# Optimization experiments

Measured on AMD Instinct MI355X. Metric: run time of the kernel, lower is better.

Reference implementation:

```python
import jax, jax.numpy as jnp
import numpy as np

B, SP, SH, H = 32, 256, 256, 512
D = 2 * H       # input feature dim (2*hidden_size)
E = H // 2      # per-liner output dim
FD = 4 * H      # fusion linear dim
EPS = 1e-13


def setup_inputs() -> dict:
    key = jax.random.key(0)
    ks = jax.random.split(key, 8)
    s = 0.02
    return dict(
        premise_batch=jax.random.normal(ks[0], (B, SP, D), jnp.float32),
        hypothesis_batch=jax.random.normal(ks[1], (B, SH, D), jnp.float32),
        premise_mask=jax.random.randint(ks[2], (B, SP), 0, 2).astype(jnp.int32),
        hypothesis_mask=jax.random.randint(ks[3], (B, SH), 0, 2).astype(jnp.int32),
        W8=jax.random.normal(ks[4], (8, D, E), jnp.float32) * s,   # liner1..8 weights (in,out)
        B8=jnp.zeros((8, E), jnp.float32),
        Wl=jax.random.normal(ks[5], (8 * E, FD), jnp.float32) * s,  # self.liner
        bl=jnp.zeros((FD,), jnp.float32),
        Wp=jax.random.normal(ks[6], (7 * D, H), jnp.float32) * s,   # self._projection
        bp=jnp.zeros((H,), jnp.float32),
    )


def masked_softmax(logits, mask):
    # ESIM-style: multiply logits by mask, softmax, re-mask, renormalize.
    m = mask[:, None, :]                        # (b,1,kv)
    r = jax.nn.softmax(logits * m, axis=-1) * m
    return r / (r.sum(axis=-1, keepdims=True) + EPS)


def fuse(x, imp_self, imp_inter, W8, B8, Wl, bl):
    # x: (b,s,D); imp_*: (b,s,1). Eight modulated views -> liner1..8 -> concat -> liner+ReLU.
    a1 = imp_self * imp_inter
    a2 = imp_self + imp_inter
    a3 = jnp.maximum(imp_self, imp_inter)
    x1 = x * imp_self
    x2 = x * imp_inter
    mx = jnp.maximum(x1, x2)
    feats = jnp.stack([x * a1, x * a2, x * a3, mx,
                       x * (a1 + 1.0), x * (a2 + 1.0), x * (a3 + 1.0), mx + x], 0)  # (8,b,s,D)
    h = jnp.einsum('kbsd,kde->kbse', feats, W8) + B8[:, None, None, :]              # (8,b,s,E)
    cat = jnp.moveaxis(h, 0, 2).reshape(x.shape[0], x.shape[1], 8 * E)              # concat order 1..8
    return jax.nn.relu(cat @ Wl + bl)           # dropout is identity in eval mode


def reference(premise_batch, hypothesis_batch, premise_mask, hypothesis_mask,
              W8, B8, Wl, bl, Wp, bp):
    pm = premise_mask.astype(jnp.float32)
    hm = hypothesis_mask.astype(jnp.float32)
    scale = 1.0 / jnp.sqrt(jnp.float32(premise_batch.shape[-1]))

    sim = jnp.einsum('bpd,bhd->bph', premise_batch, hypothesis_batch) * scale
    ph = masked_softmax(sim, hm)                               # (b,Sp,Sh)
    hp = masked_softmax(sim.transpose(0, 2, 1), pm)            # (b,Sh,Sp)
    att_p = jnp.einsum('bph,bhd->bpd', ph, hypothesis_batch) * pm[:, :, None]
    att_h = jnp.einsum('bhp,bpd->bhd', hp, premise_batch) * hm[:, :, None]

    sp_attn = jax.nn.softmax(jnp.einsum('bpd,bqd->bpq', premise_batch, premise_batch) * scale, axis=-1)
    sh_attn = jax.nn.softmax(jnp.einsum('bpd,bqd->bpq', hypothesis_batch, hypothesis_batch) * scale, axis=-1)
    self_p = sp_attn @ premise_batch
    self_h = sh_attn @ hypothesis_batch

    imp_p = sp_attn.sum(axis=-2)[..., None]        # (b,Sp,1)
    imp_h = sh_attn.sum(axis=-2)[..., None]        # (b,Sh,1)
    inter_imp_h = ph.sum(axis=-2)[..., None]       # (b,Sh,1)
    inter_imp_p = hp.sum(axis=-2)[..., None]       # (b,Sp,1)

    p_all = fuse(premise_batch, imp_p, inter_imp_p, W8, B8, Wl, bl)
    h_all = fuse(hypothesis_batch, imp_h, inter_imp_h, W8, B8, Wl, bl)

    enh_p = jnp.concatenate([premise_batch, att_p, self_p, p_all,
                             premise_batch * att_p, premise_batch - att_p], axis=-1)
    enh_h = jnp.concatenate([hypothesis_batch, att_h, self_h, h_all,
                             hypothesis_batch * att_h, hypothesis_batch - att_h], axis=-1)
    out_p = jax.nn.relu(enh_p @ Wp + bp)
    out_h = jax.nn.relu(enh_h @ Wp + bp)
    return out_p, out_h
```

## Files before the change

kernel.cpp:

```cpp
#include <hip/hip_runtime.h>
#include <hip/hip_bf16.h>
#include <cmath>

#define BB 32
#define SS 256
#define DD 1024
#define EE 256
#define FDIM 2048
#define HH 512
#define KOUT6 (6 * 1024)
#define NROW (BB * SS)
#define NROW2 (2 * NROW)

static constexpr float SCALE = 1.0f / 32.0f;
static constexpr float EPSF  = 1e-13f;

typedef __attribute__((ext_vector_type(8))) short bf16x8;
typedef __attribute__((ext_vector_type(4))) float f32x4;

__device__ inline float4 ld4(const float* p) { return *(const float4*)p; }
__device__ inline ushort f2b(float f) {
    uint x = __float_as_uint(f);
    x += 0x7fffu + ((x >> 16) & 1u);
    return (ushort)(x >> 16);
}
__device__ inline float b2f(ushort u) { return __uint_as_float(((uint)u) << 16); }
__device__ inline bf16x8 cvt8(const float* v) {
    bf16x8 r;
#pragma unroll
    for (int j = 0; j < 8; ++j) r[j] = (short)f2b(v[j]);
    return r;
}
__device__ inline void b2f8(bf16x8 v, float* o) {
#pragma unroll
    for (int j = 0; j < 8; ++j) o[j] = b2f((ushort)v[j]);
}
__device__ inline bf16x8 ldf8(const float* p) {
    const float4 u0 = ld4(p), u1 = ld4(p + 4);
    float v[8] = {u0.x, u0.y, u0.z, u0.w, u1.x, u1.y, u1.z, u1.w};
    return cvt8(v);
}

__device__ inline int swz_orig_2d() {
    const int n   = blockIdx.y * gridDim.x + blockIdx.x;
    const int tot = gridDim.x * gridDim.y;
    return (n & 7) * (tot >> 3) + (n >> 3);
}
__device__ inline int swz_orig_3d() {
    const int n   = (blockIdx.z * gridDim.y + blockIdx.y) * gridDim.x + blockIdx.x;
    const int tot = gridDim.x * gridDim.y * gridDim.z;
    return (n & 7) * (tot >> 3) + (n >> 3);
}

__global__ __launch_bounds__(256)
void tpose_cvt_k(const float* __restrict__ in, ushort* __restrict__ out,
                 int K, int N, size_t inStride, size_t outStride) {
    __shared__ float T[32][33];
    const float* ib = in  + (size_t)blockIdx.z * inStride;
    ushort*      ob = out + (size_t)blockIdx.z * outStride;
    const int k0 = blockIdx.x * 32, n0 = blockIdx.y * 32;
    const int tx = threadIdx.x & 31, ty = threadIdx.x >> 5;
#pragma unroll
    for (int i = 0; i < 4; ++i) T[ty + 8 * i][tx] = ib[(size_t)(k0 + ty + 8 * i) * N + n0 + tx];
    __syncthreads();
#pragma unroll
    for (int i = 0; i < 4; ++i)
        ob[(size_t)(n0 + ty + 8 * i) * K + k0 + tx] = f2b(T[tx][ty + 8 * i]);
}

__global__ __launch_bounds__(256)
void tpose_wp_k(const float* __restrict__ Wp, ushort* __restrict__ out) {
    __shared__ float T[32][33];
    const int k0 = blockIdx.x * 32, n0 = blockIdx.y * 32;
    const int tx = threadIdx.x & 31, ty = threadIdx.x >> 5;
#pragma unroll
    for (int i = 0; i < 4; ++i) {
        const int k = k0 + ty + 8 * i, n = n0 + tx;
        float v = Wp[(size_t)k * HH + n];
        if (k < DD)           v += Wp[(size_t)(k + 6 * DD) * HH + n];
        else if (k < 2 * DD)  v -= Wp[(size_t)(k + 5 * DD) * HH + n];
        T[ty + 8 * i][tx] = v;
    }
    __syncthreads();
#pragma unroll
    for (int i = 0; i < 4; ++i)
        out[(size_t)(n0 + ty + 8 * i) * KOUT6 + k0 + tx] = f2b(T[tx][ty + 8 * i]);
}

__global__ __launch_bounds__(256)
void prep_xprod_k(const float* __restrict__ P, const float* __restrict__ H,
                  const ushort* __restrict__ attAb,
                  ushort* __restrict__ Xb, ushort* __restrict__ prodb) {
    const int idx = blockIdx.x * 256 + threadIdx.x;
    const int row = idx >> 7, chunk = idx & 127;
    const size_t off = (size_t)row * DD + chunk * 8;
    const float* X = (row < NROW) ? (P + off) : (H + off - (size_t)NROW * DD);
    const float4 x0 = ld4(X), x1 = ld4(X + 4);
    float xv[8] = {x0.x, x0.y, x0.z, x0.w, x1.x, x1.y, x1.z, x1.w};
    float av[8];
    b2f8(*(const bf16x8*)&attAb[off], av);
    float pv[8];
#pragma unroll
    for (int j = 0; j < 8; ++j) pv[j] = xv[j] * av[j];
    *(bf16x8*)&Xb[off]    = cvt8(xv);
    *(bf16x8*)&prodb[off] = cvt8(pv);
}

__global__ __launch_bounds__(256)
void reduce_out_k(float* __restrict__ out, const float* __restrict__ p1,
                  const float* __restrict__ bp) {
    const int gid = blockIdx.x * 256 + threadIdx.x;
    const size_t o = (size_t)gid * 4;
    const float4 a = ld4(&out[o]);
    const float4 b = ld4(&p1[o]);
    const float4 bv = ld4(&bp[(int)(o & 511)]);
    *(float4*)&out[o] = make_float4(fmaxf(a.x + b.x + bv.x, 0.f),
                                    fmaxf(a.y + b.y + bv.y, 0.f),
                                    fmaxf(a.z + b.z + bv.z, 0.f),
                                    fmaxf(a.w + b.w + bv.w, 0.f));
}

__global__ __launch_bounds__(256)
void softmax4_k(float* __restrict__ simPH, float* __restrict__ simPHT,
                float* __restrict__ simPP, float* __restrict__ simHH,
                const int* __restrict__ pma, const int* __restrict__ hma) {
    const int job = blockIdx.y;
    float* buf = job == 0 ? simPH : job == 1 ? simPHT : job == 2 ? simPP : simHH;
    const int* mask = job == 0 ? hma : job == 1 ? pma : nullptr;
    __shared__ float  redm[4];
    __shared__ float2 reds[4];
    const int row = blockIdx.x;
    const int b   = row >> 8;
    const int j   = threadIdx.x;
    const float v = buf[(size_t)row * SS + j];
    float mj = 1.0f, z = v;
    if (mask) { mj = (float)mask[b * SS + j]; z = v * mj; }
    float M = z;
#pragma unroll
    for (int off = 1; off < 64; off <<= 1) M = fmaxf(M, __shfl_xor(M, off));
    const int wid = j >> 6;
    if ((j & 63) == 0) redm[wid] = M;
    __syncthreads();
    M = fmaxf(fmaxf(redm[0], redm[1]), fmaxf(redm[2], redm[3]));
    const float e = expf(z - M);
    const float r = e * mj;
    float sz = e, sr = r;
#pragma unroll
    for (int off = 1; off < 64; off <<= 1) {
        sz += __shfl_xor(sz, off);
        sr += __shfl_xor(sr, off);
    }
    if ((j & 63) == 0) reds[wid] = make_float2(sz, sr);
    __syncthreads();
    const float Z  = reds[0].x + reds[1].x + reds[2].x + reds[3].x;
    const float Sm = reds[0].y + reds[1].y + reds[2].y + reds[3].y;
    buf[(size_t)row * SS + j] = mask ? (r / (Sm + EPSF * Z)) : (e / Z);
}

__global__ __launch_bounds__(256)
void colsum4_k(const float* __restrict__ spA, const float* __restrict__ shA,
               const float* __restrict__ hp, const float* __restrict__ ph,
               float* __restrict__ impS, float* __restrict__ impI) {
    const int job = blockIdx.y, b = blockIdx.x, j = threadIdx.x;
    const float* src = job == 0 ? spA : job == 1 ? shA : job == 2 ? hp : ph;
    float* dst = job == 0 ? impS : job == 1 ? impS + NROW : job == 2 ? impI : impI + NROW;
    const float* Mb = src + (size_t)b * SS * SS;
    float s = 0.f;
    for (int i = 0; i < SS; ++i) s += Mb[i * SS + j];
    dst[b * SS + j] = s;
}

#define LSWZ(kg, r) ((r) ^ ((kg) << 1))

#define MFMA_CORE()                                                                  \
    {                                                                                \
        bf16x8 afr[4], bfr[4];                                                       \
        _Pragma("unroll") for (int m = 0; m < 4; ++m)                                \
            afr[m] = *(const bf16x8*)As[kq][LSWZ(kq, wr + m * 16 + fr)];             \
        _Pragma("unroll") for (int n = 0; n < 4; ++n)                                \
            bfr[n] = *(const bf16x8*)Bs[kq][LSWZ(kq, wc + n * 16 + fr)];             \
        _Pragma("unroll") for (int m = 0; m < 4; ++m)                                \
            _Pragma("unroll") for (int n = 0; n < 4; ++n)                            \
                acc[m][n] = __builtin_amdgcn_mfma_f32_16x16x32_bf16(                 \
                    afr[m], bfr[n], acc[m][n], 0, 0, 0);                             \
    }

#define MFMA_PREAMBLE()                                                              \
    const int tid = threadIdx.x;                                                     \
    const int lane = tid & 63;                                                       \
    const int w = tid >> 6;                                                          \
    const int wr = (w >> 1) * 64, wc = (w & 1) * 64;                                 \
    const int fr = lane & 15;                                                        \
    const int kq = lane >> 4;                                                        \
    const int rq = kq * 4;                                                           \
    f32x4 acc[4][4] = {};

__global__ __launch_bounds__(256)
void mfma_nt_k(const float* __restrict__ P, const float* __restrict__ H,
               float* __restrict__ simPH, float* __restrict__ simPHT,
               float* __restrict__ simPP, float* __restrict__ simHH) {
    __shared__ __align__(16) ushort As[4][128][8];
    __shared__ __align__(16) ushort Bs[4][128][8];
    int orig = swz_orig_3d();
    const int cb = orig & 1; orig >>= 1;
    const int rb = orig & 1; orig >>= 1;
    const int g = orig >> 5, b = orig & 31;
    const float* Au = ((g == 2) ? H : P) + (size_t)b * SS * DD;
    const float* Bu = ((g == 1) ? P : H) + (size_t)b * SS * DD;
    const int col0 = cb * 128, row0 = rb * 128;
    MFMA_PREAMBLE();
    for (int k0 = 0; k0 < DD; k0 += 32) {
        bf16x8 ar[2], br[2];
#pragma unroll
        for (int i = 0; i < 2; ++i) {
            const int cid = tid + i * 256, srow = cid >> 2, skc = (cid & 3) * 8;
            ar[i] = ldf8(&Au[(size_t)(row0 + srow) * DD + k0 + skc]);
            br[i] = ldf8(&Bu[(size_t)(col0 + srow) * DD + k0 + skc]);
        }
        __syncthreads();
#pragma unroll
        for (int i = 0; i < 2; ++i) {
            const int cid = tid + i * 256, kg = cid & 3, rr = LSWZ(kg, cid >> 2);
            *(bf16x8*)As[kg][rr] = ar[i];
            *(bf16x8*)Bs[kg][rr] = br[i];
        }
        __syncthreads();
        MFMA_CORE();
    }
    float* Cb = (g == 0 ? simPH : g == 1 ? simPP : simHH) + (size_t)b * SS * SS;
#pragma unroll
    for (int m = 0; m < 4; ++m)
#pragma unroll
        for (int n = 0; n < 4; ++n) {
            const int c = col0 + wc + n * 16 + fr;
            const int r0 = row0 + wr + m * 16 + rq;
#pragma unroll
            for (int r = 0; r < 4; ++r) Cb[(size_t)(r0 + r) * SS + c] = acc[m][n][r] * SCALE;
            if (g == 0) {
                float* Tb = simPHT + (size_t)b * SS * SS;
                *(float4*)&Tb[(size_t)c * SS + r0] =
                    make_float4(acc[m][n][0] * SCALE, acc[m][n][1] * SCALE,
                                acc[m][n][2] * SCALE, acc[m][n][3] * SCALE);
            }
        }
}

__global__ __launch_bounds__(256)
void mfma_att_k(const float* __restrict__ ph, const float* __restrict__ hp,
                const float* __restrict__ spA, const float* __restrict__ shA,
                const ushort* __restrict__ PbT, const ushort* __restrict__ HbT,
                const int* __restrict__ pma, const int* __restrict__ hma,
                ushort* __restrict__ attAb, ushort* __restrict__ selfAb) {
    __shared__ __align__(16) ushort As[4][128][8];
    __shared__ __align__(16) ushort Bs[4][128][8];
    int orig = swz_orig_3d();
    const int x = orig & 7; orig >>= 3;
    const int y = orig & 1; orig >>= 1;
    const int g = orig >> 5, b = orig & 31;
    const float*  W  = (g == 0 ? ph : g == 1 ? hp : g == 2 ? spA : shA) + (size_t)b * SS * SS;
    const ushort* BT = ((g == 0 || g == 3) ? HbT : PbT) + (size_t)b * DD * SS;
    const int* rmask = g == 0 ? pma + b * SS : g == 1 ? hma + b * SS : nullptr;
    const int side = (g == 1 || g == 3);
    ushort* Ob = (g < 2 ? attAb : selfAb) + ((size_t)side * NROW + (size_t)b * SS) * DD;
    const int col0 = x * 128, row0 = y * 128;
    MFMA_PREAMBLE();
    for (int k0 = 0; k0 < SS; k0 += 32) {
        bf16x8 ar[2], br[2];
#pragma unroll
        for (int i = 0; i < 2; ++i) {
            const int cid = tid + i * 256, srow = cid >> 2, skc = (cid & 3) * 8;
            ar[i] = ldf8(&W[(size_t)(row0 + srow) * SS + k0 + skc]);
            br[i] = *(const bf16x8*)&BT[(size_t)(col0 + srow) * SS + k0 + skc];
        }
        __syncthreads();
#pragma unroll
        for (int i = 0; i < 2; ++i) {
            const int cid = tid + i * 256, kg = cid & 3, rr = LSWZ(kg, cid >> 2);
            *(bf16x8*)As[kg][rr] = ar[i];
            *(bf16x8*)Bs[kg][rr] = br[i];
        }
        __syncthreads();
        MFMA_CORE();
    }
#pragma unroll
    for (int m = 0; m < 4; ++m)
#pragma unroll
        for (int n = 0; n < 4; ++n) {
            const int c = col0 + wc + n * 16 + fr;
#pragma unroll
            for (int r = 0; r < 4; ++r) {
                const int rr = row0 + wr + m * 16 + rq + r;
                const float mm = rmask ? (float)rmask[rr] : 1.0f;
                Ob[(size_t)rr * DD + c] = f2b(acc[m][n][r] * mm);
            }
        }
}

__global__ __launch_bounds__(256)
void mfma_fuse_k(const float* __restrict__ P, const float* __restrict__ H,
                 const float* __restrict__ impS, const float* __restrict__ impI,
                 const ushort* __restrict__ W8T, const float* __restrict__ B8v,
                 ushort* __restrict__ catb) {
    __shared__ __align__(16) ushort As[4][128][8];
    __shared__ __align__(16) ushort Bs[4][128][8];
    const int orig = swz_orig_2d();
    const int cb = orig & 15, rb = orig >> 4;
    const int kf = cb >> 1, e0 = (cb & 1) * 128, row0 = rb * 128;
    const float* X = (row0 < NROW) ? P : H;
    const int rbase = (row0 < NROW) ? row0 : row0 - NROW;
    MFMA_PREAMBLE();
    const ushort* Wk = W8T + (size_t)kf * EE * DD;

    int srow_[2]; float sA[2], iA[2], cf[2];
#pragma unroll
    for (int i = 0; i < 2; ++i) {
        const int cid = tid + i * 256;
        srow_[i] = cid >> 2;
        const float s_ = impS[row0 + srow_[i]], i_ = impI[row0 + srow_[i]];
        sA[i] = s_; iA[i] = i_;
        float c = 0.f;
        switch (kf) {
            case 0: c = s_ * i_;             break;
            case 1: c = s_ + i_;             break;
            case 2: c = fmaxf(s_, i_);       break;
            case 4: c = s_ * i_ + 1.f;       break;
            case 5: c = s_ + i_ + 1.f;       break;
            case 6: c = fmaxf(s_, i_) + 1.f; break;
            default: break;
        }
        cf[i] = c;
    }
    for (int k0 = 0; k0 < DD; k0 += 32) {
        bf16x8 ar[2], br[2];
#pragma unroll
        for (int i = 0; i < 2; ++i) {
            const int cid = tid + i * 256, skc = (cid & 3) * 8;
            const float* src = &X[(size_t)(rbase + srow_[i]) * DD + k0 + skc];
            const float4 u0 = ld4(src), u1 = ld4(src + 4);
            float v[8] = {u0.x, u0.y, u0.z, u0.w, u1.x, u1.y, u1.z, u1.w};
            if (kf == 3) {
#pragma unroll
                for (int j = 0; j < 8; ++j) v[j] = fmaxf(v[j] * sA[i], v[j] * iA[i]);
            } else if (kf == 7) {
#pragma unroll
                for (int j = 0; j < 8; ++j) v[j] = fmaxf(v[j] * sA[i], v[j] * iA[i]) + v[j];
            } else {
#pragma unroll
                for (int j = 0; j < 8; ++j) v[j] *= cf[i];
            }
            ar[i] = cvt8(v);
            br[i] = *(const bf16x8*)&Wk[(size_t)(e0 + srow_[i]) * DD + k0 + skc];
        }
        __syncthreads();
#pragma unroll
        for (int i = 0; i < 2; ++i) {
            const int cid = tid + i * 256, kg = cid & 3, rr = LSWZ(kg, cid >> 2);
            *(bf16x8*)As[kg][rr] = ar[i];
            *(bf16x8*)Bs[kg][rr] = br[i];
        }
        __syncthreads();
        MFMA_CORE();
    }
#pragma unroll
    for (int m = 0; m < 4; ++m)
#pragma unroll
        for (int n = 0; n < 4; ++n) {
            const int el = e0 + wc + n * 16 + fr;
            const float bv = B8v[kf * EE + el];
#pragma unroll
            for (int r = 0; r < 4; ++r) {
                const int rr = row0 + wr + m * 16 + rq + r;
                catb[(size_t)rr * FDIM + kf * EE + el] = f2b(acc[m][n][r] + bv);
            }
        }
}

__global__ __launch_bounds__(256)
void mfma_lin_k(const ushort* __restrict__ A, const ushort* __restrict__ BT,
                const float* __restrict__ bias, ushort* __restrict__ C) {
    __shared__ __align__(16) ushort As[4][128][8];
    __shared__ __align__(16) ushort Bs[4][128][8];
    const int orig = swz_orig_2d();
    const int col0 = (orig & 15) * 128, row0 = (orig >> 4) * 128;
    MFMA_PREAMBLE();
    for (int k0 = 0; k0 < FDIM; k0 += 32) {
        bf16x8 ar[2], br[2];
#pragma unroll
        for (int i = 0; i < 2; ++i) {
            const int cid = tid + i * 256, srow = cid >> 2, skc = (cid & 3) * 8;
            ar[i] = *(const bf16x8*)&A [(size_t)(row0 + srow) * FDIM + k0 + skc];
            br[i] = *(const bf16x8*)&BT[(size_t)(col0 + srow) * FDIM + k0 + skc];
        }
        __syncthreads();
#pragma unroll
        for (int i = 0; i < 2; ++i) {
            const int cid = tid + i * 256, kg = cid & 3, rr = LSWZ(kg, cid >> 2);
            *(bf16x8*)As[kg][rr] = ar[i];
            *(bf16x8*)Bs[kg][rr] = br[i];
        }
        __syncthreads();
        MFMA_CORE();
    }
#pragma unroll
    for (int m = 0; m < 4; ++m)
#pragma unroll
        for (int n = 0; n < 4; ++n) {
            const int c = col0 + wc + n * 16 + fr;
            const float bv = bias[c];
#pragma unroll
            for (int r = 0; r < 4; ++r) {
                const int rr = row0 + wr + m * 16 + rq + r;
                C[(size_t)rr * FDIM + c] = f2b(fmaxf(acc[m][n][r] + bv, 0.f));
            }
        }
}

__device__ inline void out_seg(int k0, const ushort* Xb, const ushort* attAb,
                               const ushort* selfAb, const ushort* pallb,
                               const ushort* prodb,
                               const ushort*& seg, int& pitch, int& kloc) {
    switch (k0 >> 10) {
        case 0:  seg = Xb;     pitch = DD;   kloc = k0;          break;
        case 1:  seg = attAb;  pitch = DD;   kloc = k0 - DD;     break;
        case 2:  seg = selfAb; pitch = DD;   kloc = k0 - 2 * DD; break;
        case 3:
        case 4:  seg = pallb;  pitch = FDIM; kloc = k0 - 3 * DD; break;
        default: seg = prodb;  pitch = DD;   kloc = k0 - 5 * DD; break;
    }
}

__global__ __launch_bounds__(256)
void mfma_out_k(const ushort* __restrict__ Xb, const ushort* __restrict__ attAb,
                const ushort* __restrict__ selfAb, const ushort* __restrict__ pallb,
                const ushort* __restrict__ prodb, const ushort* __restrict__ WpT,
                const float* __restrict__ bp, float* __restrict__ dst0,
                float* __restrict__ dst1, int kchunk, int finalize) {
    __shared__ __align__(16) ushort As[4][128][8];
    __shared__ __align__(16) ushort Bs[4][128][8];
    int orig = swz_orig_3d();
    const int x = orig & 3; orig >>= 2;
    const int y = orig & 127; orig >>= 7;
    const int z = orig;
    const int col0 = x * 128, row0 = y * 128;
    const int kbase = z * kchunk;
    float* dst = z == 0 ? dst0 : dst1;
    MFMA_PREAMBLE();
    for (int t = 0; t < kchunk / 32; ++t) {
        const int k0 = kbase + t * 32;
        const ushort* seg; int pitch, kloc;
        out_seg(k0, Xb, attAb, selfAb, pallb, prodb, seg, pitch, kloc);
        bf16x8 ar[2], br[2];
#pragma unroll
        for (int i = 0; i < 2; ++i) {
            const int cid = tid + i * 256, srow = cid >> 2, skc = (cid & 3) * 8;
            ar[i] = *(const bf16x8*)&seg[(size_t)(row0 + srow) * pitch + kloc + skc];
            br[i] = *(const bf16x8*)&WpT[(size_t)(col0 + srow) * KOUT6 + k0 + skc];
        }
        __syncthreads();
#pragma unroll
        for (int i = 0; i < 2; ++i) {
            const int cid = tid + i * 256, kg = cid & 3, rr = LSWZ(kg, cid >> 2);
            *(bf16x8*)As[kg][rr] = ar[i];
            *(bf16x8*)Bs[kg][rr] = br[i];
        }
        __syncthreads();
        MFMA_CORE();
    }
#pragma unroll
    for (int m = 0; m < 4; ++m)
#pragma unroll
        for (int n = 0; n < 4; ++n) {
            const int c = col0 + wc + n * 16 + fr;
            const float bv = finalize ? bp[c] : 0.f;
#pragma unroll
            for (int r = 0; r < 4; ++r) {
                const int rr = row0 + wr + m * 16 + rq + r;
                const float v = acc[m][n][r] + bv;
                dst[(size_t)rr * HH + c] = finalize ? fmaxf(v, 0.f) : v;
            }
        }
}

extern "C" void kernel_launch(void* const* d_in, const int* in_sizes, int n_in,
                              void* d_out, int out_size, void* d_ws, size_t ws_size,
                              hipStream_t stream) {
    const float* P   = (const float*)d_in[0];
    const float* Hb  = (const float*)d_in[1];
    const int*   pma = (const int*)d_in[2];
    const int*   hma = (const int*)d_in[3];
    const float* W8  = (const float*)d_in[4];
    const float* B8v = (const float*)d_in[5];
    const float* Wl  = (const float*)d_in[6];
    const float* bl  = (const float*)d_in[7];
    const float* Wp  = (const float*)d_in[8];
    const float* bp  = (const float*)d_in[9];

    char* base = (char*)d_ws;
    float* simPH  = (float*)base;
    float* simPHT = simPH  + (size_t)BB * SS * SS;
    float* simPP  = simPHT + (size_t)BB * SS * SS;
    float* simHH  = simPP  + (size_t)BB * SS * SS;
    ushort* PbT   = (ushort*)(simHH + (size_t)BB * SS * SS);
    ushort* HbT   = PbT + (size_t)NROW * DD;
    ushort* catb  = (ushort*)base;
    ushort* Xb    = (ushort*)base;
    ushort* prodb = Xb + (size_t)NROW2 * DD;
    char* cur = (char*)(HbT + (size_t)NROW * DD);
    auto alloc_f = [&](size_t n) { float*  p = (float*)cur;  cur += n * 4; return p; };
    auto alloc_u = [&](size_t n) { ushort* p = (ushort*)cur; cur += n * 2; return p; };
    float*  impS   = alloc_f(NROW2);
    float*  impI   = alloc_f(NROW2);
    ushort* attAb  = alloc_u((size_t)NROW2 * DD);
    ushort* selfAb = alloc_u((size_t)NROW2 * DD);
    ushort* pallb  = alloc_u((size_t)NROW2 * FDIM);
    ushort* WlT    = alloc_u((size_t)FDIM * FDIM);
    ushort* WpT    = alloc_u((size_t)HH * KOUT6);
    ushort* W8T    = alloc_u((size_t)8 * EE * DD);
    float*  part1  = alloc_f((size_t)NROW2 * HH);

    const size_t need_split = (size_t)((char*)(part1 + (size_t)NROW2 * HH) - base);
    const bool split = ws_size >= need_split;

    float* outp = (float*)d_out;
    const dim3 blk(256);

    tpose_cvt_k<<<dim3(8, 32, BB), blk, 0, stream>>>(P,  PbT, SS, DD, (size_t)SS * DD, (size_t)DD * SS);
    tpose_cvt_k<<<dim3(8, 32, BB), blk, 0, stream>>>(Hb, HbT, SS, DD, (size_t)SS * DD, (size_t)DD * SS);
    tpose_cvt_k<<<dim3(FDIM / 32, FDIM / 32, 1), blk, 0, stream>>>(Wl, WlT, FDIM, FDIM, 0, 0);
    tpose_wp_k<<<dim3(KOUT6 / 32, HH / 32, 1), blk, 0, stream>>>(Wp, WpT);
    tpose_cvt_k<<<dim3(DD / 32, EE / 32, 8), blk, 0, stream>>>(W8, W8T, DD, EE,
                                                               (size_t)DD * EE, (size_t)EE * DD);

    mfma_nt_k<<<dim3(2, 2, 96), blk, 0, stream>>>(P, Hb, simPH, simPHT, simPP, simHH);
    softmax4_k<<<dim3(NROW, 4), blk, 0, stream>>>(simPH, simPHT, simPP, simHH, pma, hma);
    colsum4_k<<<dim3(BB, 4), blk, 0, stream>>>(simPP, simHH, simPHT, simPH, impS, impI);
    mfma_att_k<<<dim3(8, 2, 128), blk, 0, stream>>>(simPH, simPHT, simPP, simHH, PbT, HbT,
                                                    pma, hma, attAb, selfAb);

    mfma_fuse_k<<<dim3(16, 128), blk, 0, stream>>>(P, Hb, impS, impI, W8T, B8v, catb);
    mfma_lin_k<<<dim3(16, 128), blk, 0, stream>>>(catb, WlT, bl, pallb);
    prep_xprod_k<<<dim3(NROW2 * DD / 8 / 256), blk, 0, stream>>>(P, Hb, attAb, Xb, prodb);
    if (split) {
        mfma_out_k<<<dim3(4, 128, 2), blk, 0, stream>>>(Xb, attAb, selfAb, pallb, prodb,
                                                        WpT, bp, outp, part1, KOUT6 / 2, 0);
        reduce_out_k<<<dim3(NROW2 * HH / 4 / 256), blk, 0, stream>>>(outp, part1, bp);
    } else {
        mfma_out_k<<<dim3(4, 128, 1), blk, 0, stream>>>(Xb, attAb, selfAb, pallb, prodb,
                                                        WpT, bp, outp, outp, KOUT6, 1);
    }

    (void)in_sizes; (void)n_in; (void)out_size; (void)ws_size;
}
```

Measured before the change: 762.0 us.

## Store similarity/attention matrices in bf16 and split column-sum into two passes

The four 256x256 similarity/attention buffers are now written by the NT GEMM as bf16 instead of fp32. Softmax reads and writes them in bf16 with one wave per row and no shared-memory reductions, and the attention GEMM loads them directly as bf16 fragments. The serial column-sum kernel, which had only 128 blocks each looping over 256 rows, is replaced by a partial-sum pass over 8 row chunks followed by a small reduction pass, giving more parallelism. This cuts memory traffic and conversion work. In exchange, the logits are rounded to bf16 before softmax and the column sums read rounded probabilities, which lowers precision.

```diff
diff --git a/kernel.cpp b/kernel.cpp
--- a/kernel.cpp
+++ b/kernel.cpp
@@ -11,6 +11,7 @@
 #define KOUT6 (6 * 1024)
 #define NROW (BB * SS)
 #define NROW2 (2 * NROW)
+#define SIMSZ ((size_t)BB * SS * SS)
 
 static constexpr float SCALE = 1.0f / 32.0f;
 static constexpr float EPSF  = 1e-13f;
@@ -121,52 +122,74 @@
 }
 
 __global__ __launch_bounds__(256)
-void softmax4_k(float* __restrict__ simPH, float* __restrict__ simPHT,
-                float* __restrict__ simPP, float* __restrict__ simHH,
+void softmax4_k(ushort* __restrict__ simPH, ushort* __restrict__ simPHT,
+                ushort* __restrict__ simPP, ushort* __restrict__ simHH,
                 const int* __restrict__ pma, const int* __restrict__ hma) {
     const int job = blockIdx.y;
-    float* buf = job == 0 ? simPH : job == 1 ? simPHT : job == 2 ? simPP : simHH;
+    ushort* buf = job == 0 ? simPH : job == 1 ? simPHT : job == 2 ? simPP : simHH;
     const int* mask = job == 0 ? hma : job == 1 ? pma : nullptr;
-    __shared__ float  redm[4];
-    __shared__ float2 reds[4];
-    const int row = blockIdx.x;
-    const int b   = row >> 8;
-    const int j   = threadIdx.x;
-    const float v = buf[(size_t)row * SS + j];
-    float mj = 1.0f, z = v;
-    if (mask) { mj = (float)mask[b * SS + j]; z = v * mj; }
-    float M = z;
+    const int w = threadIdx.x >> 6, lane = threadIdx.x & 63;
+    const int row = blockIdx.x * 4 + w;
+    const int b = row >> 8;
+    ushort* rp = buf + (size_t)row * SS + lane * 4;
+    ushort4 u = *(const ushort4*)rp;
+    float z[4], mj[4];
+    const ushort uv[4] = {u.x, u.y, u.z, u.w};
+#pragma unroll
+    for (int c = 0; c < 4; ++c) {
+        const float v = b2f(uv[c]);
+        float m = 1.f;
+        if (mask) m = (float)mask[b * SS + lane * 4 + c];
+        mj[c] = m; z[c] = v * m;
+    }
+    float M = fmaxf(fmaxf(z[0], z[1]), fmaxf(z[2], z[3]));
 #pragma unroll
     for (int off = 1; off < 64; off <<= 1) M = fmaxf(M, __shfl_xor(M, off));
-    const int wid = j >> 6;
-    if ((j & 63) == 0) redm[wid] = M;
-    __syncthreads();
-    M = fmaxf(fmaxf(redm[0], redm[1]), fmaxf(redm[2], redm[3]));
-    const float e = expf(z - M);
-    const float r = e * mj;
-    float sz = e, sr = r;
+    float e[4], r[4], sz = 0.f, sr = 0.f;
+#pragma unroll
+    for (int c = 0; c < 4; ++c) {
+        e[c] = expf(z[c] - M);
+        r[c] = e[c] * mj[c];
+        sz += e[c]; sr += r[c];
+    }
 #pragma unroll
     for (int off = 1; off < 64; off <<= 1) {
         sz += __shfl_xor(sz, off);
         sr += __shfl_xor(sr, off);
     }
-    if ((j & 63) == 0) reds[wid] = make_float2(sz, sr);
-    __syncthreads();
-    const float Z  = reds[0].x + reds[1].x + reds[2].x + reds[3].x;
-    const float Sm = reds[0].y + reds[1].y + reds[2].y + reds[3].y;
-    buf[(size_t)row * SS + j] = mask ? (r / (Sm + EPSF * Z)) : (e / Z);
-}
-
-__global__ __launch_bounds__(256)
-void colsum4_k(const float* __restrict__ spA, const float* __restrict__ shA,
-               const float* __restrict__ hp, const float* __restrict__ ph,
-               float* __restrict__ impS, float* __restrict__ impI) {
+    ushort4 o;
+    if (mask) {
+        const float d = 1.f / (sr + EPSF * sz);
+        o.x = f2b(r[0] * d); o.y = f2b(r[1] * d); o.z = f2b(r[2] * d); o.w = f2b(r[3] * d);
+    } else {
+        const float d = 1.f / sz;
+        o.x = f2b(e[0] * d); o.y = f2b(e[1] * d); o.z = f2b(e[2] * d); o.w = f2b(e[3] * d);
+    }
+    *(ushort4*)rp = o;
+}
+
+__global__ __launch_bounds__(256)
+void colsum_p1_k(const ushort* __restrict__ simPP, const ushort* __restrict__ simHH,
+                 const ushort* __restrict__ simPHT, const ushort* __restrict__ simPH,
+                 float* __restrict__ pbuf) {
+    const int job = blockIdx.y, b = blockIdx.x, rc = blockIdx.z, j = threadIdx.x;
+    const ushort* src = job == 0 ? simPP : job == 1 ? simHH : job == 2 ? simPHT : simPH;
+    const ushort* Mb = src + (size_t)b * SS * SS + (size_t)rc * 32 * SS;
+    float s = 0.f;
+#pragma unroll 4
+    for (int i = 0; i < 32; ++i) s += b2f(Mb[i * SS + j]);
+    pbuf[(((size_t)job * BB + b) * 8 + rc) * SS + j] = s;
+}
+
+__global__ __launch_bounds__(256)
+void colsum_p2_k(const float* __restrict__ pbuf,
+                 float* __restrict__ impS, float* __restrict__ impI) {
     const int job = blockIdx.y, b = blockIdx.x, j = threadIdx.x;
-    const float* src = job == 0 ? spA : job == 1 ? shA : job == 2 ? hp : ph;
+    const float* pb = pbuf + ((size_t)job * BB + b) * 8 * SS;
+    float s = 0.f;
+#pragma unroll
+    for (int rc = 0; rc < 8; ++rc) s += pb[rc * SS + j];
     float* dst = job == 0 ? impS : job == 1 ? impS + NROW : job == 2 ? impI : impI + NROW;
-    const float* Mb = src + (size_t)b * SS * SS;
-    float s = 0.f;
-    for (int i = 0; i < SS; ++i) s += Mb[i * SS + j];
     dst[b * SS + j] = s;
 }
 
@@ -197,8 +220,8 @@
 
 __global__ __launch_bounds__(256)
 void mfma_nt_k(const float* __restrict__ P, const float* __restrict__ H,
-               float* __restrict__ simPH, float* __restrict__ simPHT,
-               float* __restrict__ simPP, float* __restrict__ simHH) {
+               ushort* __restrict__ simPH, ushort* __restrict__ simPHT,
+               ushort* __restrict__ simPP, ushort* __restrict__ simHH) {
     __shared__ __align__(16) ushort As[4][128][8];
     __shared__ __align__(16) ushort Bs[4][128][8];
     int orig = swz_orig_3d();
@@ -227,7 +250,7 @@
         __syncthreads();
         MFMA_CORE();
     }
-    float* Cb = (g == 0 ? simPH : g == 1 ? simPP : simHH) + (size_t)b * SS * SS;
+    ushort* Cb = (g == 0 ? simPH : g == 1 ? simPP : simHH) + (size_t)b * SS * SS;
 #pragma unroll
     for (int m = 0; m < 4; ++m)
 #pragma unroll
@@ -235,19 +258,20 @@
             const int c = col0 + wc + n * 16 + fr;
             const int r0 = row0 + wr + m * 16 + rq;
 #pragma unroll
-            for (int r = 0; r < 4; ++r) Cb[(size_t)(r0 + r) * SS + c] = acc[m][n][r] * SCALE;
+            for (int r = 0; r < 4; ++r) Cb[(size_t)(r0 + r) * SS + c] = f2b(acc[m][n][r] * SCALE);
             if (g == 0) {
-                float* Tb = simPHT + (size_t)b * SS * SS;
-                *(float4*)&Tb[(size_t)c * SS + r0] =
-                    make_float4(acc[m][n][0] * SCALE, acc[m][n][1] * SCALE,
-                                acc[m][n][2] * SCALE, acc[m][n][3] * SCALE);
+                ushort* Tb = simPHT + (size_t)b * SS * SS;
+                ushort4 t;
+                t.x = f2b(acc[m][n][0] * SCALE); t.y = f2b(acc[m][n][1] * SCALE);
+                t.z = f2b(acc[m][n][2] * SCALE); t.w = f2b(acc[m][n][3] * SCALE);
+                *(ushort4*)&Tb[(size_t)c * SS + r0] = t;
             }
         }
 }
 
 __global__ __launch_bounds__(256)
-void mfma_att_k(const float* __restrict__ ph, const float* __restrict__ hp,
-                const float* __restrict__ spA, const float* __restrict__ shA,
+void mfma_att_k(const ushort* __restrict__ ph, const ushort* __restrict__ hp,
+                const ushort* __restrict__ spA, const ushort* __restrict__ shA,
                 const ushort* __restrict__ PbT, const ushort* __restrict__ HbT,
                 const int* __restrict__ pma, const int* __restrict__ hma,
                 ushort* __restrict__ attAb, ushort* __restrict__ selfAb) {
@@ -257,7 +281,7 @@
     const int x = orig & 7; orig >>= 3;
     const int y = orig & 1; orig >>= 1;
     const int g = orig >> 5, b = orig & 31;
-    const float*  W  = (g == 0 ? ph : g == 1 ? hp : g == 2 ? spA : shA) + (size_t)b * SS * SS;
+    const ushort* W  = (g == 0 ? ph : g == 1 ? hp : g == 2 ? spA : shA) + (size_t)b * SS * SS;
     const ushort* BT = ((g == 0 || g == 3) ? HbT : PbT) + (size_t)b * DD * SS;
     const int* rmask = g == 0 ? pma + b * SS : g == 1 ? hma + b * SS : nullptr;
     const int side = (g == 1 || g == 3);
@@ -269,7 +293,7 @@
 #pragma unroll
         for (int i = 0; i < 2; ++i) {
             const int cid = tid + i * 256, srow = cid >> 2, skc = (cid & 3) * 8;
-            ar[i] = ldf8(&W[(size_t)(row0 + srow) * SS + k0 + skc]);
+            ar[i] = *(const bf16x8*)&W [(size_t)(row0 + srow) * SS + k0 + skc];
             br[i] = *(const bf16x8*)&BT[(size_t)(col0 + srow) * SS + k0 + skc];
         }
         __syncthreads();
@@ -496,16 +520,16 @@
     const float* bp  = (const float*)d_in[9];
 
     char* base = (char*)d_ws;
-    float* simPH  = (float*)base;
-    float* simPHT = simPH  + (size_t)BB * SS * SS;
-    float* simPP  = simPHT + (size_t)BB * SS * SS;
-    float* simHH  = simPP  + (size_t)BB * SS * SS;
-    ushort* PbT   = (ushort*)(simHH + (size_t)BB * SS * SS);
-    ushort* HbT   = PbT + (size_t)NROW * DD;
-    ushort* catb  = (ushort*)base;
-    ushort* Xb    = (ushort*)base;
-    ushort* prodb = Xb + (size_t)NROW2 * DD;
-    char* cur = (char*)(HbT + (size_t)NROW * DD);
+    ushort* simPH  = (ushort*)base;
+    ushort* simPHT = simPH  + SIMSZ;
+    ushort* simPP  = simPHT + SIMSZ;
+    ushort* simHH  = simPP  + SIMSZ;
+    ushort* PbT    = simHH + SIMSZ;
+    ushort* HbT    = PbT + (size_t)NROW * DD;
+    ushort* catb   = (ushort*)base;
+    ushort* Xb     = (ushort*)base;
+    ushort* prodb  = Xb + (size_t)NROW2 * DD;
+    char* cur = base + (size_t)NROW2 * FDIM * 2;
     auto alloc_f = [&](size_t n) { float*  p = (float*)cur;  cur += n * 4; return p; };
     auto alloc_u = [&](size_t n) { ushort* p = (ushort*)cur; cur += n * 2; return p; };
     float*  impS   = alloc_f(NROW2);
@@ -516,6 +540,7 @@
     ushort* WlT    = alloc_u((size_t)FDIM * FDIM);
     ushort* WpT    = alloc_u((size_t)HH * KOUT6);
     ushort* W8T    = alloc_u((size_t)8 * EE * DD);
+    float*  pbuf   = alloc_f((size_t)4 * BB * 8 * SS);
     float*  part1  = alloc_f((size_t)NROW2 * HH);
 
     const size_t need_split = (size_t)((char*)(part1 + (size_t)NROW2 * HH) - base);
@@ -532,8 +557,9 @@
                                                                (size_t)DD * EE, (size_t)EE * DD);
 
     mfma_nt_k<<<dim3(2, 2, 96), blk, 0, stream>>>(P, Hb, simPH, simPHT, simPP, simHH);
-    softmax4_k<<<dim3(NROW, 4), blk, 0, stream>>>(simPH, simPHT, simPP, simHH, pma, hma);
-    colsum4_k<<<dim3(BB, 4), blk, 0, stream>>>(simPP, simHH, simPHT, simPH, impS, impI);
+    softmax4_k<<<dim3(NROW / 4, 4), blk, 0, stream>>>(simPH, simPHT, simPP, simHH, pma, hma);
+    colsum_p1_k<<<dim3(BB, 4, 8), blk, 0, stream>>>(simPP, simHH, simPHT, simPH, pbuf);
+    colsum_p2_k<<<dim3(BB, 4), blk, 0, stream>>>(pbuf, impS, impI);
     mfma_att_k<<<dim3(8, 2, 128), blk, 0, stream>>>(simPH, simPHT, simPP, simHH, PbT, HbT,
                                                     pma, hma, attAb, selfAb);
 
```

New measurement: 726.8 us. 1.05x faster.
